# Performance work log

Hardware: AMD Instinct MI355X
Metric: run time of the kernel (lower is better)

Reference implementation:

```python
import math
import jax, jax.numpy as jnp
from jax import lax
import numpy as np

B, N, D, H, L, F = 128, 200, 128, 8, 3, 2048


def setup_inputs():
    key = jax.random.key(0)
    ks = jax.random.split(key, 24)
    g = lambda i, shape: (0.05 * jax.random.normal(ks[i], shape)).astype(jnp.float32)
    coords = jax.random.uniform(ks[0], (B, N, 2), dtype=jnp.float32)
    demands = jax.random.uniform(ks[1], (B, N), minval=1.0, maxval=10.0, dtype=jnp.float32)
    demands = demands.at[:, 0].set(0.0)  # depot demand = 0
    capacity = jnp.full((B,), 50.0, jnp.float32)
    return dict(
        coords=coords, demands_raw=demands, capacity_raw=capacity,
        embed_W=g(2, (D, 3)), embed_b=g(3, (D,)),
        Wqkv=g(4, (L, 3 * D, D)), bqkv=g(5, (L, 3 * D)),
        Wo=g(6, (L, D, D)), bo=g(7, (L, D)),
        W1=g(8, (L, F, D)), b1=g(9, (L, F)),
        W2=g(10, (L, D, F)), b2=g(11, (L, D)),
        ln1_g=jnp.ones((L, D), jnp.float32), ln1_b=jnp.zeros((L, D), jnp.float32),
        ln2_g=jnp.ones((L, D), jnp.float32), ln2_b=jnp.zeros((L, D), jnp.float32),
        Wq=g(12, (D, D)), Wk=g(13, (D, D)),
        Wcap=g(14, (D, 1)), bcap=g(15, (D,)),
        Wctx=g(16, (D, 3 * D)), bctx=g(17, (D,)),
    )


def _ln(x, g, b):
    m = x.mean(-1, keepdims=True)
    v = ((x - m) ** 2).mean(-1, keepdims=True)
    return (x - m) / jnp.sqrt(v + 1e-5) * g + b


def _forward(coords, demands_raw, capacity_raw, embed_W, embed_b, Wqkv, bqkv, Wo, bo,
             W1, b1, W2, b2, ln1_g, ln1_b, ln2_g, ln2_b, Wq, Wk, Wcap, bcap, Wctx, bctx):
    Bd, Nd, _ = coords.shape
    cap = capacity_raw.reshape(Bd, 1)
    demand_ratio = demands_raw / cap                       # (B,N)
    x = jnp.concatenate([coords, demand_ratio[..., None]], -1)  # (B,N,3)
    h = x @ embed_W.T + embed_b                            # (B,N,D)
    d = h.shape[-1]
    dh = d // H
    # --- transformer encoder (post-LN, relu FFN), eval mode (no dropout) ---
    for i in range(Wqkv.shape[0]):
        qkv = h @ Wqkv[i].T + bqkv[i]
        q, k, v = jnp.split(qkv, 3, -1)
        q = q.reshape(Bd, Nd, H, dh)
        k = k.reshape(Bd, Nd, H, dh)
        v = v.reshape(Bd, Nd, H, dh)
        s = jnp.einsum('bqhd,bkhd->bhqk', q, k) / math.sqrt(dh)
        a = jax.nn.softmax(s, -1)
        o = jnp.einsum('bhqk,bkhd->bqhd', a, v).reshape(Bd, Nd, d) @ Wo[i].T + bo[i]
        h = _ln(h + o, ln1_g[i], ln1_b[i])
        f = jax.nn.relu(h @ W1[i].T + b1[i]) @ W2[i].T + b2[i]
        h = _ln(h + f, ln2_g[i], ln2_b[i])
    global_ctx = h.mean(1)                                 # (B,D)
    kmat = h @ Wk.T                                        # K cache: static across steps
    sqrt_d = math.sqrt(d)
    max_steps = 2 * (Nd - 1) + 1
    ar = jnp.arange(Bd)

    def step(carry, _):
        current, visited, remaining, done, key = carry
        key, sk = jax.random.split(key)
        cur_h = h[ar, current]                             # (B,D)
        cap_h = remaining @ Wcap.T + bcap                  # (B,D)
        q_in = jnp.concatenate([cur_h, global_ctx, cap_h], -1)
        q = (q_in @ Wctx.T + bctx) @ Wq.T                  # (B,D)
        logits = (kmat * q[:, None, :]).sum(-1) / sqrt_d   # (B,N)
        infeasible = visited | (demand_ratio > remaining)
        feas_cust = (~visited[:, 1:]) & (demand_ratio[:, 1:] <= remaining)
        has_feas = feas_cust.any(1)
        all_served = visited[:, 1:].all(1)
        force_depot = all_served & (current != 0) & (~done)
        at_depot = (current == 0) & (~done)
        not_depot = (current != 0) & (~done)
        # prevent_early_return=True path
        depot_mask = (at_depot & has_feas) | (not_depot & has_feas & (~all_served))
        infeasible = infeasible.at[:, 0].set(infeasible[:, 0] | depot_mask)
        force_depot = force_depot | (not_depot & (~has_feas)) | done
        masked = jnp.where(infeasible, -1e9, logits)
        logp = jax.nn.log_softmax(masked, -1)
        sel = jax.random.categorical(sk, masked)           # sampling decode
        sel_logp = logp[ar, sel]
        sel = jnp.where(force_depot, 0, sel)
        sel_logp = jnp.where(force_depot, 0.0, sel_logp)
        is_depot = sel == 0
        take = demand_ratio[ar, sel][:, None]
        remaining = jnp.clip(jnp.where(is_depot[:, None], 1.0, remaining - take), 0.0, 1.0)
        visited = visited.at[ar, sel].set(visited[ar, sel] | (~is_depot))
        done = done | (visited[:, 1:].all(1) & (sel == 0))
        return (sel, visited, remaining, done, key), (sel, sel_logp)

    init = (jnp.zeros(Bd, jnp.int32), jnp.zeros((Bd, Nd), bool),
            jnp.ones((Bd, 1), coords.dtype), jnp.zeros(Bd, bool), jax.random.key(42))
    _, (acts, lps) = lax.scan(step, init, None, length=max_steps)
    path = jnp.concatenate([jnp.zeros((Bd, 1), jnp.int32), acts.T], 1)  # (B, 1+max_steps)
    logps = lps.sum(0)                                                  # (B,)
    return path, logps


def reference(coords, demands_raw, capacity_raw, embed_W, embed_b, Wqkv, bqkv, Wo, bo,
              W1, b1, W2, b2, ln1_g, ln1_b, ln2_g, ln2_b, Wq, Wk, Wcap, bcap, Wctx, bctx):
    return _forward(coords, demands_raw, capacity_raw, embed_W, embed_b, Wqkv, bqkv, Wo, bo,
                    W1, b1, W2, b2, ln1_g, ln1_b, ln2_g, ln2_b, Wq, Wk, Wcap, bcap, Wctx, bctx)
```

## Files before the change

kernel.cpp:

```cpp
#include <hip/hip_runtime.h>
#include <hip/hip_bf16.h>
#include <stdint.h>
#include <math.h>

#define NB 128
#define NN 200
#define ND 128
#define NH 8
#define DH 16
#define NL 3
#define NF 2048
#define NT (NB * NN)
#define NSTEP 399

__host__ __device__ inline void tf2x32(unsigned k0, unsigned k1, unsigned x0, unsigned x1,
                                       unsigned* o0, unsigned* o1) {
  unsigned ks[3] = {k0, k1, k0 ^ k1 ^ 0x1BD11BDAu};
  x0 += ks[0]; x1 += ks[1];
  const unsigned R[2][4] = {{13u, 15u, 26u, 6u}, {17u, 29u, 16u, 24u}};
#pragma unroll
  for (int i = 0; i < 5; ++i) {
#pragma unroll
    for (int j = 0; j < 4; ++j) {
      unsigned r = R[i & 1][j];
      x0 += x1;
      x1 = (x1 << r) | (x1 >> (32u - r));
      x1 ^= x0;
    }
    x0 += ks[(i + 1) % 3];
    x1 += ks[(i + 2) % 3] + (unsigned)(i + 1);
  }
  *o0 = x0; *o1 = x1;
}

__global__ void k_rng(unsigned* __restrict__ rng) {
  unsigned k0 = 0u, k1 = 42u;
  for (int t = 0; t < NSTEP; ++t) {
    unsigned a0, a1, s0, s1;
    tf2x32(k0, k1, 0u, 1u, &s0, &s1);
    tf2x32(k0, k1, 0u, 0u, &a0, &a1);
    rng[2 * t] = s0; rng[2 * t + 1] = s1;
    k0 = a0; k1 = a1;
  }
}

__global__ __launch_bounds__(256) void k_gum(const unsigned* __restrict__ rng, float* __restrict__ gum) {
  int idx = blockIdx.x * 256 + threadIdx.x;
  if (idx >= NSTEP * NT) return;
  int t = idx / NT, j = idx - t * NT;
  unsigned o0, o1;
  tf2x32(rng[2 * t], rng[2 * t + 1], 0u, (unsigned)j, &o0, &o1);
  unsigned bits = o0 ^ o1;
  float u01 = __uint_as_float((bits >> 9) | 0x3f800000u) - 1.0f;
  float uu = fmaxf(1.17549435082228751e-38f, u01);
  gum[idx] = (float)(-log(-log((double)uu)));
}

__global__ void k_tr(const float* __restrict__ src, float* __restrict__ dst, int R, int C) {
  int i = blockIdx.x * 256 + threadIdx.x;
  if (i >= R * C) return;
  int c = i / R, r = i - c * R;
  dst[i] = src[(size_t)r * C + c];
}

__global__ void k_trd(const float* __restrict__ src, double* __restrict__ dst, int R, int C) {
  int i = blockIdx.x * 256 + threadIdx.x;
  if (i >= R * C) return;
  int c = i / R, r = i - c * R;
  dst[i] = (double)src[(size_t)r * C + c];
}

__global__ void k_embed(const float* __restrict__ coords, const float* __restrict__ dem,
                        const float* __restrict__ cap, const float* __restrict__ eW,
                        const float* __restrict__ eb, float* __restrict__ h, float* __restrict__ dr) {
  int gid = blockIdx.x * blockDim.x + threadIdx.x;
  int t = gid >> 7, d = gid & 127;
  int b = t / NN;
  float drv = dem[t] / cap[b];
  double acc = (double)eW[d * 3] * (double)coords[2 * t]
             + (double)eW[d * 3 + 1] * (double)coords[2 * t + 1]
             + (double)eW[d * 3 + 2] * (double)drv;
  h[gid] = (float)acc + eb[d];
  if (d == 0) dr[t] = drv;
}

#define QT 8
__global__ __launch_bounds__(384) void k_qkv(const float* __restrict__ h, const double* __restrict__ WT,
                                             const float* __restrict__ bias, float* __restrict__ qkv) {
  const int t0 = blockIdx.x * QT, j = threadIdx.x;
  __shared__ double hsh[ND][QT];
  for (int idx = j; idx < ND * QT; idx += 384) {
    int t = idx & 7, k = idx >> 3;
    hsh[k][t] = (double)h[(size_t)(t0 + t) * ND + k];
  }
  __syncthreads();
  double acc[QT];
#pragma unroll
  for (int t = 0; t < QT; ++t) acc[t] = 0.0;
  for (int k = 0; k < ND; ++k) {
    double w = WT[(size_t)k * 384 + j];
#pragma unroll
    for (int t = 0; t < QT; ++t) acc[t] += w * hsh[k][t];
  }
  float bv = bias[j];
#pragma unroll
  for (int t = 0; t < QT; ++t)
    qkv[(size_t)(t0 + t) * 384 + j] = (float)acc[t] + bv;
}

__global__ __launch_bounds__(256) void k_attn(const float* __restrict__ qkv, float* __restrict__ att) {
  const int b = blockIdx.x / NH, hh = blockIdx.x % NH, tid = threadIdx.x;
  const int lane = tid & 63, w = tid >> 6;
  __shared__ float qsh[NN][DH + 1];
  __shared__ float ksh[NN][DH + 1];
  __shared__ float vsh[NN][DH + 1];
  __shared__ float ashw[4][NN + 8];
  for (int idx = tid; idx < NN * DH; idx += 256) {
    int n = idx / DH, d2 = idx % DH;
    size_t base = (size_t)(b * NN + n) * 384 + hh * DH + d2;
    qsh[n][d2] = qkv[base];
    ksh[n][d2] = qkv[base + ND];
    vsh[n][d2] = qkv[base + 2 * ND];
  }
  __syncthreads();
  const int dd = lane & 15, q4 = lane >> 4;
  for (int qn = w; qn < NN; qn += 4) {
    double qv[DH];
#pragma unroll
    for (int d = 0; d < DH; ++d) qv[d] = (double)qsh[qn][d];
    float sf[4];
#pragma unroll
    for (int s = 0; s < 4; ++s) {
      int n = lane + 64 * s;
      if (n < NN) {
        double a = 0.0;
#pragma unroll
        for (int d = 0; d < DH; ++d) a += qv[d] * (double)ksh[n][d];
        sf[s] = (float)a / 4.0f;
      } else sf[s] = -3.0e38f;
    }
    float m = fmaxf(fmaxf(sf[0], sf[1]), fmaxf(sf[2], sf[3]));
    for (int off = 1; off < 64; off <<= 1) m = fmaxf(m, __shfl_xor(m, off, 64));
    double e[4];
    double esum = 0.0;
#pragma unroll
    for (int s = 0; s < 4; ++s) {
      int n = lane + 64 * s;
      e[s] = (n < NN) ? exp((double)(sf[s] - m)) : 0.0;
      esum += e[s];
    }
    for (int off = 1; off < 64; off <<= 1) esum += __shfl_xor(esum, off, 64);
#pragma unroll
    for (int s = 0; s < 4; ++s) {
      int n = lane + 64 * s;
      if (n < NN) ashw[w][n] = (float)(e[s] / esum);
    }
    double o = 0.0;
    for (int i = 0; i < 50; ++i) {
      int n = q4 * 50 + i;
      o += (double)ashw[w][n] * (double)vsh[n][dd];
    }
    o += __shfl_xor(o, 16, 64);
    o += __shfl_xor(o, 32, 64);
    if (lane < DH)
      att[(size_t)(b * NN + qn) * ND + hh * DH + lane] = (float)o;
  }
}

#define OT 4
__global__ __launch_bounds__(128) void k_oln(const float* __restrict__ att, const double* __restrict__ WoT,
                                             const float* __restrict__ bo, const float* __restrict__ g,
                                             const float* __restrict__ bb, float* __restrict__ h) {
  const int t0 = blockIdx.x * OT, d = threadIdx.x;
  __shared__ double ash[ND][OT];
  __shared__ float xsh[OT][ND];
  __shared__ float mred[OT], sred[OT];
  for (int idx = d; idx < ND * OT; idx += 128) {
    int t = idx & 3, k = idx >> 2;
    ash[k][t] = (double)att[(size_t)(t0 + t) * ND + k];
  }
  __syncthreads();
  double acc[OT];
#pragma unroll
  for (int t = 0; t < OT; ++t) acc[t] = 0.0;
  for (int k = 0; k < ND; ++k) {
    double w = WoT[(size_t)k * ND + d];
#pragma unroll
    for (int t = 0; t < OT; ++t) acc[t] += w * ash[k][t];
  }
  float bv = bo[d];
#pragma unroll
  for (int t = 0; t < OT; ++t) {
    float o = (float)acc[t] + bv;
    xsh[t][d] = h[(size_t)(t0 + t) * ND + d] + o;
  }
  __syncthreads();
  if (d < OT) {
    double sv = 0.0;
    for (int k = 0; k < ND; ++k) sv += (double)xsh[d][k];
    float m = (float)(sv / 128.0);
    double sq = 0.0;
    for (int k = 0; k < ND; ++k) { float tf = xsh[d][k] - m; sq += (double)tf * (double)tf; }
    mred[d] = m;
    sred[d] = sqrtf((float)(sq / 128.0) + 1e-5f);
  }
  __syncthreads();
#pragma unroll
  for (int t = 0; t < OT; ++t) {
    float tf = xsh[t][d] - mred[t];
    h[(size_t)(t0 + t) * ND + d] = tf / sred[t] * g[d] + bb[d];
  }
}

#define FT 8
#define JC 1024
__global__ __launch_bounds__(256) void k_ffn(float* __restrict__ h, const double* __restrict__ W1T,
                                             const float* __restrict__ b1, const float* __restrict__ W2T,
                                             const float* __restrict__ b2, const float* __restrict__ g,
                                             const float* __restrict__ bb) {
  const int t0 = blockIdx.x * FT, tid = threadIdx.x;
  __shared__ double hsh[ND][FT];
  __shared__ double fsh[FT][JC];
  __shared__ float xsh[FT][ND];
  __shared__ float mred[FT], sred[FT];
  for (int idx = tid; idx < ND * FT; idx += 256) {
    int t = idx & 7, k = idx >> 3;
    hsh[k][t] = (double)h[(size_t)(t0 + t) * ND + k];
  }
  __syncthreads();
  const int jg = tid >> 5, dl = tid & 31;
  double acc2[4][FT];
#pragma unroll
  for (int a = 0; a < 4; ++a)
#pragma unroll
    for (int t = 0; t < FT; ++t) acc2[a][t] = 0.0;
  for (int c = 0; c < 2; ++c) {
    {
      const int j0 = tid * 4;
      double acc[4][FT];
#pragma unroll
      for (int a = 0; a < 4; ++a)
#pragma unroll
        for (int t = 0; t < FT; ++t) acc[a][t] = 0.0;
      for (int k = 0; k < ND; ++k) {
        double hv[FT];
#pragma unroll
        for (int t = 0; t < FT; ++t) hv[t] = hsh[k][t];
        const double* wp = W1T + (size_t)k * NF + c * JC + j0;
        double2 wa = *(const double2*)wp;
        double2 wb = *(const double2*)(wp + 2);
        double wd[4] = {wa.x, wa.y, wb.x, wb.y};
#pragma unroll
        for (int a = 0; a < 4; ++a)
#pragma unroll
          for (int t = 0; t < FT; ++t) acc[a][t] += wd[a] * hv[t];
      }
#pragma unroll
      for (int a = 0; a < 4; ++a) {
        float bv = b1[c * JC + j0 + a];
#pragma unroll
        for (int t = 0; t < FT; ++t) {
          float f = (float)acc[a][t] + bv;
          fsh[t][j0 + a] = (double)fmaxf(f, 0.0f);
        }
      }
    }
    __syncthreads();
    for (int i = 0; i < 128; ++i) {
      int jj = (jg << 7) | ((i + jg) & 127);
      int j = c * JC + jj;
      double fv[FT];
#pragma unroll
      for (int t = 0; t < FT; ++t) fv[t] = fsh[t][jj];
      float4 wv = *(const float4*)(W2T + (size_t)j * ND + (dl << 2));
      double wd[4] = {(double)wv.x, (double)wv.y, (double)wv.z, (double)wv.w};
#pragma unroll
      for (int a = 0; a < 4; ++a)
#pragma unroll
        for (int t = 0; t < FT; ++t) acc2[a][t] += wd[a] * fv[t];
    }
    __syncthreads();
  }
  double* red = &fsh[0][0];
#pragma unroll
  for (int a = 0; a < 4; ++a)
#pragma unroll
    for (int t = 0; t < FT; ++t)
      red[(((jg * 8 + t) << 7)) + (dl << 2) + a] = acc2[a][t];
  __syncthreads();
  for (int idx = tid; idx < ND * FT; idx += 256) {
    int t = idx >> 7, d = idx & 127;
    double s = 0.0;
#pragma unroll
    for (int jg2 = 0; jg2 < 8; ++jg2) s += red[((jg2 * 8 + t) << 7) + d];
    float o = (float)s + b2[d];
    float hf = (float)hsh[d][t];
    xsh[t][d] = hf + o;
  }
  __syncthreads();
  if (tid < FT) {
    double sv = 0.0;
    for (int d = 0; d < ND; ++d) sv += (double)xsh[tid][d];
    float m = (float)(sv / 128.0);
    double sq = 0.0;
    for (int d = 0; d < ND; ++d) { float tf = xsh[tid][d] - m; sq += (double)tf * (double)tf; }
    mred[tid] = m;
    sred[tid] = sqrtf((float)(sq / 128.0) + 1e-5f);
  }
  __syncthreads();
  for (int idx = tid; idx < ND * FT; idx += 256) {
    int d = idx & 127, t = idx >> 7;
    float tf = xsh[t][d] - mred[t];
    h[(size_t)(t0 + t) * ND + d] = tf / sred[t] * g[d] + bb[d];
  }
}

__global__ __launch_bounds__(128) void k_gctx(const float* __restrict__ h, float* __restrict__ gctx) {
  int b = blockIdx.x, d = threadIdx.x;
  double acc = 0.0;
  for (int n = 0; n < NN; ++n) acc += (double)h[(size_t)(b * NN + n) * ND + d];
  gctx[b * ND + d] = (float)(acc / 200.0);
}

#define KT 8
__global__ __launch_bounds__(128) void k_kmat(const float* __restrict__ h, const double* __restrict__ WkT,
                                              float* __restrict__ kmat) {
  const int t0 = blockIdx.x * KT, d = threadIdx.x;
  __shared__ double hsh[ND][KT];
  for (int idx = d; idx < ND * KT; idx += 128) {
    int t = idx & 7, k = idx >> 3;
    hsh[k][t] = (double)h[(size_t)(t0 + t) * ND + k];
  }
  __syncthreads();
  double acc[KT];
#pragma unroll
  for (int t = 0; t < KT; ++t) acc[t] = 0.0;
  for (int k = 0; k < ND; ++k) {
    double w = WkT[(size_t)k * ND + d];
#pragma unroll
    for (int t = 0; t < KT; ++t) acc[t] += w * hsh[k][t];
  }
#pragma unroll
  for (int t = 0; t < KT; ++t)
    kmat[(size_t)(t0 + t) * ND + d] = (float)acc[t];
}

__global__ __launch_bounds__(128) void k_prep1(const float* __restrict__ Wctx, const float* __restrict__ bcap,
                                               const float* __restrict__ Wcap, const float* __restrict__ bctx,
                                               double* __restrict__ t1, double* __restrict__ wu) {
  int k = threadIdx.x;
  double a = 0.0, c = 0.0;
  for (int m = 0; m < ND; ++m) {
    double wc = (double)Wctx[(size_t)k * 384 + 256 + m];
    a += wc * (double)bcap[m];
    c += wc * (double)Wcap[m];
  }
  t1[k] = a + (double)bctx[k];
  wu[k] = c;
}

__global__ __launch_bounds__(128) void k_M(const float* __restrict__ Wq, const float* __restrict__ Wctx,
                                           double* __restrict__ M) {
  int d = blockIdx.x, j = threadIdx.x;
  double acc = 0.0;
  for (int k = 0; k < ND; ++k)
    acc += (double)Wq[(size_t)d * ND + k] * (double)Wctx[(size_t)k * 384 + j];
  M[(size_t)d * ND + j] = acc;
}

__global__ __launch_bounds__(128) void k_u(const float* __restrict__ Wq, const double* __restrict__ wu,
                                           double* __restrict__ u) {
  int d = threadIdx.x;
  double acc = 0.0;
  for (int k = 0; k < ND; ++k) acc += (double)Wq[(size_t)d * ND + k] * wu[k];
  u[d] = acc;
}

__global__ __launch_bounds__(128) void k_t2(const float* __restrict__ Wctx, const float* __restrict__ gctx,
                                            double* __restrict__ t2) {
  int b = blockIdx.x, k = threadIdx.x;
  double acc = 0.0;
  for (int m = 0; m < ND; ++m)
    acc += (double)Wctx[(size_t)k * 384 + 128 + m] * (double)gctx[b * ND + m];
  t2[(size_t)b * ND + k] = acc;
}

__global__ __launch_bounds__(128) void k_vb(const float* __restrict__ Wq, const double* __restrict__ t2,
                                            const double* __restrict__ t1, double* __restrict__ vb) {
  int b = blockIdx.x, d = threadIdx.x;
  double acc = 0.0;
  for (int k = 0; k < ND; ++k)
    acc += (double)Wq[(size_t)d * ND + k] * (t2[(size_t)b * ND + k] + t1[k]);
  vb[(size_t)b * ND + d] = acc;
}

__global__ __launch_bounds__(256) void k_c01(const float* __restrict__ kmat, const double* __restrict__ vb,
                                             const double* __restrict__ u, float* __restrict__ c0, float* __restrict__ c1) {
  int t = blockIdx.x * 256 + threadIdx.x;
  if (t >= NT) return;
  int b = t / NN;
  double a0 = 0.0, a1 = 0.0;
  for (int d = 0; d < ND; ++d) {
    double km = (double)kmat[(size_t)t * ND + d];
    a0 += km * vb[(size_t)b * ND + d];
    a1 += km * u[d];
  }
  c0[t] = (float)a0;
  c1[t] = (float)a1;
}

__global__ __launch_bounds__(128) void k_KM(const float* __restrict__ kmat, const double* __restrict__ M,
                                            float* __restrict__ KMT) {
  const int t0 = blockIdx.x * KT, j = threadIdx.x;
  const int b = t0 / NN, toff = t0 % NN;
  __shared__ double ksh[ND][KT];
  for (int idx = j; idx < ND * KT; idx += 128) {
    int t = idx & 7, k = idx >> 3;
    ksh[k][t] = (double)kmat[(size_t)(t0 + t) * ND + k];
  }
  __syncthreads();
  double acc[KT];
#pragma unroll
  for (int t = 0; t < KT; ++t) acc[t] = 0.0;
  for (int d = 0; d < ND; ++d) {
    double m = M[(size_t)d * ND + j];
#pragma unroll
    for (int t = 0; t < KT; ++t) acc[t] += ksh[d][t] * m;
  }
#pragma unroll
  for (int t = 0; t < KT; ++t)
    KMT[(size_t)b * ND * NN + (size_t)j * NN + toff + t] = (float)acc[t];
}

#define PC 8
__global__ __launch_bounds__(256) void k_P(const float* __restrict__ KMT, const float* __restrict__ h,
                                           float* __restrict__ P) {
  const int blk = blockIdx.x;
  const int b = blk / 25, c0 = (blk % 25) * PC;
  const int tid = threadIdx.x;
  __shared__ double h8[ND][PC];
  for (int idx = tid; idx < ND * PC; idx += 256) {
    int t = idx & 7, j = idx >> 3;
    h8[j][t] = (double)h[(size_t)(b * NN + c0 + t) * ND + j];
  }
  __syncthreads();
  if (tid < NN) {
    double acc[PC];
#pragma unroll
    for (int t = 0; t < PC; ++t) acc[t] = 0.0;
    const float* kb = KMT + (size_t)b * ND * NN + tid;
    for (int j = 0; j < ND; ++j) {
      double km = (double)kb[(size_t)j * NN];
#pragma unroll
      for (int t = 0; t < PC; ++t) acc[t] += km * h8[j][t];
    }
#pragma unroll
    for (int t = 0; t < PC; ++t)
      P[(size_t)(b * NN + c0 + t) * NN + tid] = (float)acc[t];
  }
}

__global__ __launch_bounds__(64) void k_decode(const float* __restrict__ P, const float* __restrict__ c0,
                                               const float* __restrict__ c1, const float* __restrict__ dr,
                                               const float* __restrict__ gum, float* __restrict__ out) {
  __shared__ float Psh[NN * NN];
  const int b = blockIdx.x, l = threadIdx.x;
  {
    const float4* src = (const float4*)(P + (size_t)b * NN * NN);
    float4* dst = (float4*)Psh;
    for (int i = l; i < (NN * NN) / 4; i += 64) dst[i] = src[i];
  }
  float drs4[4], c04[4], c14[4];
  int vis4[4];
#pragma unroll
  for (int s = 0; s < 4; ++s) {
    int n = l + 64 * s;
    bool valid = n < NN;
    drs4[s] = valid ? dr[b * NN + n] : 1e9f;
    c04[s] = valid ? c0[b * NN + n] : 0.0f;
    c14[s] = valid ? c1[b * NN + n] : 0.0f;
    vis4[s] = valid ? 0 : 1;
  }
  int cur = 0, done = 0;
  float rem = 1.0f, lpsum = 0.0f;
  if (l == 0) out[(size_t)b * 400] = 0.0f;
  __syncthreads();
  const float SQD = 11.3137084989847603f;
  float gv4[4];
#pragma unroll
  for (int s = 0; s < 4; ++s) {
    int n = l + 64 * s;
    gv4[s] = (n < NN) ? gum[(size_t)0 * NT + b * NN + n] : 0.0f;
  }
  for (int t = 0; t < NSTEP; ++t) {
    float gn4[4];
    if (t + 1 < NSTEP) {
      const float* grow = gum + (size_t)(t + 1) * NT + b * NN;
#pragma unroll
      for (int s = 0; s < 4; ++s) {
        int n = l + 64 * s;
        gn4[s] = (n < NN) ? grow[n] : 0.0f;
      }
    }
    const float* Prow = Psh + cur * NN;
    float Pv4[4];
#pragma unroll
    for (int s = 0; s < 4; ++s) {
      int n = l + 64 * s;
      Pv4[s] = (n < NN) ? Prow[n] : 0.0f;
    }
    bool lf = false, lns = false;
#pragma unroll
    for (int s = 0; s < 4; ++s) {
      int n = l + 64 * s;
      if (n >= 1 && n < NN && !vis4[s]) {
        lns = true;
        if (drs4[s] <= rem) lf = true;
      }
    }
    const int has_feas = (__ballot(lf) != 0ULL);
    const int all_served = (__ballot(lns) == 0ULL);
    const bool at_depot = (cur == 0) && !done, not_depot = (cur != 0) && !done;
    const bool depot_mask = (at_depot && has_feas) || (not_depot && has_feas && !all_served);
    float msk[4], sc[4];
#pragma unroll
    for (int s = 0; s < 4; ++s) {
      int n = l + 64 * s;
      if (n < NN) {
        double sd = (double)Pv4[s] + (double)c04[s] + (double)rem * (double)c14[s];
        float logit = (float)sd / SQD;
        bool infn = vis4[s] || (drs4[s] > rem) || (n == 0 && depot_mask);
        msk[s] = infn ? -1e9f : logit;
        sc[s] = msk[s] + gv4[s];
      } else {
        msk[s] = -3.0e38f;
        sc[s] = -3.0e38f;
      }
    }
    float bs = sc[0]; int bn = l; float bmsk = msk[0]; float mx = msk[0];
#pragma unroll
    for (int s = 1; s < 4; ++s) {
      int n = l + 64 * s;
      if (sc[s] > bs) { bs = sc[s]; bn = n; bmsk = msk[s]; }
      mx = fmaxf(mx, msk[s]);
    }
    for (int off = 1; off < 64; off <<= 1) {
      float os = __shfl_xor(bs, off, 64);
      int on = __shfl_xor(bn, off, 64);
      float ob = __shfl_xor(bmsk, off, 64);
      float om = __shfl_xor(mx, off, 64);
      if (os > bs || (os == bs && on < bn)) { bs = os; bn = on; bmsk = ob; }
      mx = fmaxf(mx, om);
    }
    float e = 0.0f;
#pragma unroll
    for (int s = 0; s < 4; ++s) e += expf(msk[s] - mx);
    for (int off = 1; off < 64; off <<= 1) e += __shfl_xor(e, off, 64);
    int sel = bn;
    float slp = (bmsk - mx) - logf(e);
    bool force = (all_served && cur != 0 && !done) || (not_depot && !has_feas) || done;
    if (force) { sel = 0; slp = 0.0f; }
    if (l == 0) out[(size_t)b * 400 + 1 + t] = (float)sel;
    lpsum += slp;
    bool isd = (sel == 0);
    float cand = drs4[sel >> 6];
    float take = __shfl(cand, sel & 63, 64);
    float nr = isd ? 1.0f : (rem - take);
    rem = fminf(fmaxf(nr, 0.0f), 1.0f);
    if (!isd && (sel & 63) == l) vis4[sel >> 6] = 1;
    if (all_served && sel == 0) done = 1;
    cur = sel;
#pragma unroll
    for (int s = 0; s < 4; ++s) gv4[s] = gn4[s];
  }
  if (l == 0) out[(size_t)NB * 400 + b] = lpsum;
}

extern "C" void kernel_launch(void* const* d_in, const int* in_sizes, int n_in,
                              void* d_out, int out_size, void* d_ws, size_t ws_size,
                              hipStream_t stream) {
  (void)in_sizes; (void)n_in; (void)out_size; (void)ws_size;
  const float* coords = (const float*)d_in[0];
  const float* dem    = (const float*)d_in[1];
  const float* cap    = (const float*)d_in[2];
  const float* eW     = (const float*)d_in[3];
  const float* eb     = (const float*)d_in[4];
  const float* Wqkv   = (const float*)d_in[5];
  const float* bqkv   = (const float*)d_in[6];
  const float* Wo     = (const float*)d_in[7];
  const float* bo     = (const float*)d_in[8];
  const float* W1     = (const float*)d_in[9];
  const float* b1     = (const float*)d_in[10];
  const float* W2     = (const float*)d_in[11];
  const float* b2     = (const float*)d_in[12];
  const float* ln1g   = (const float*)d_in[13];
  const float* ln1b   = (const float*)d_in[14];
  const float* ln2g   = (const float*)d_in[15];
  const float* ln2b   = (const float*)d_in[16];
  const float* Wq     = (const float*)d_in[17];
  const float* Wk     = (const float*)d_in[18];
  const float* Wcap   = (const float*)d_in[19];
  const float* bcap   = (const float*)d_in[20];
  const float* Wctx   = (const float*)d_in[21];
  const float* bctx   = (const float*)d_in[22];

  char* ws = (char*)d_ws;
  size_t off = 0;
  auto take = [&](size_t bytes) -> void* {
    void* p = ws + off;
    off += (bytes + 255) & ~(size_t)255;
    return p;
  };
  float* dr   = (float*)take((size_t)NT * 4);
  float* c0   = (float*)take((size_t)NT * 4);
  float* c1   = (float*)take((size_t)NT * 4);
  float* P    = (float*)take((size_t)NB * NN * NN * 4);
  unsigned* rng = (unsigned*)take((size_t)NSTEP * 2 * 4);
  float* h    = (float*)take((size_t)NT * ND * 4);
  float* qkv  = (float*)take((size_t)NT * 384 * 4);
  float* att  = (float*)take((size_t)NT * ND * 4);
  float* kmat = (float*)take((size_t)NT * ND * 4);
  float* gctx = (float*)take((size_t)NB * ND * 4);
  double* M   = (double*)take((size_t)ND * ND * 8);
  double* u   = (double*)take((size_t)ND * 8);
  double* t1  = (double*)take((size_t)ND * 8);
  double* wu  = (double*)take((size_t)ND * 8);
  double* t2  = (double*)take((size_t)NB * ND * 8);
  double* vb  = (double*)take((size_t)NB * ND * 8);
  double* W1T   = (double*)take((size_t)NL * NF * ND * 8);
  float*  W2T   = (float*)take((size_t)NL * NF * ND * 4);
  double* WqkvT = (double*)take((size_t)NL * 384 * ND * 8);
  double* WoT   = (double*)take((size_t)NL * ND * ND * 8);
  double* WkT   = (double*)take((size_t)ND * ND * 8);
  float* KMT = qkv;
  float* gum = h;

  k_rng<<<1, 1, 0, stream>>>(rng);
  for (int i = 0; i < NL; ++i) {
    k_trd<<<(NF * ND + 255) / 256, 256, 0, stream>>>(W1 + (size_t)i * NF * ND, W1T + (size_t)i * NF * ND, NF, ND);
    k_tr<<<(NF * ND + 255) / 256, 256, 0, stream>>>(W2 + (size_t)i * ND * NF, W2T + (size_t)i * ND * NF, ND, NF);
    k_trd<<<(384 * ND + 255) / 256, 256, 0, stream>>>(Wqkv + (size_t)i * 384 * ND, WqkvT + (size_t)i * 384 * ND, 384, ND);
    k_trd<<<(ND * ND + 255) / 256, 256, 0, stream>>>(Wo + (size_t)i * ND * ND, WoT + (size_t)i * ND * ND, ND, ND);
  }
  k_trd<<<(ND * ND + 255) / 256, 256, 0, stream>>>(Wk, WkT, ND, ND);
  k_embed<<<(NT * ND) / 256, 256, 0, stream>>>(coords, dem, cap, eW, eb, h, dr);
  for (int i = 0; i < NL; ++i) {
    k_qkv<<<NT / QT, 384, 0, stream>>>(h, WqkvT + (size_t)i * 384 * ND, bqkv + (size_t)i * 384, qkv);
    k_attn<<<NB * NH, 256, 0, stream>>>(qkv, att);
    k_oln<<<NT / OT, 128, 0, stream>>>(att, WoT + (size_t)i * ND * ND, bo + (size_t)i * ND,
                                       ln1g + (size_t)i * ND, ln1b + (size_t)i * ND, h);
    k_ffn<<<NT / FT, 256, 0, stream>>>(h, W1T + (size_t)i * NF * ND, b1 + (size_t)i * NF,
                                       W2T + (size_t)i * ND * NF, b2 + (size_t)i * ND,
                                       ln2g + (size_t)i * ND, ln2b + (size_t)i * ND);
  }
  k_gctx<<<NB, 128, 0, stream>>>(h, gctx);
  k_kmat<<<NT / KT, 128, 0, stream>>>(h, WkT, kmat);
  k_prep1<<<1, 128, 0, stream>>>(Wctx, bcap, Wcap, bctx, t1, wu);
  k_M<<<ND, 128, 0, stream>>>(Wq, Wctx, M);
  k_u<<<1, 128, 0, stream>>>(Wq, wu, u);
  k_t2<<<NB, 128, 0, stream>>>(Wctx, gctx, t2);
  k_vb<<<NB, 128, 0, stream>>>(Wq, t2, t1, vb);
  k_c01<<<NT / 256, 256, 0, stream>>>(kmat, vb, u, c0, c1);
  k_KM<<<NT / KT, 128, 0, stream>>>(kmat, M, KMT);
  k_P<<<NB * 25, 256, 0, stream>>>(KMT, h, P);
  k_gum<<<(NSTEP * NT + 255) / 256, 256, 0, stream>>>(rng, gum);
  k_decode<<<NB, 64, 0, stream>>>(P, c0, c1, dr, gum, (float*)d_out);
}
```

Measured before the change: 4.746 ms.

## Halve FFN shared memory, prefetch FFN weights, parallelize RNG key splitting

The FFN kernel now stores the ReLU intermediate in shared memory as float instead of double, halving that buffer (64KB to 32KB), and splits the cross-group reduction into two halves so it fits in the smaller buffer. This should allow more blocks to be resident per CU. Both FFN inner loops software-prefetch the next weight row into registers to hide global-load latency, at the cost of extra registers. The RNG kernel computes the sequential key chain on one thread and then spreads the per-step subkey derivation across 64 threads.

Result: no change. 4.747 ms (+0.0%).

```diff
diff --git a/kernel.cpp b/kernel.cpp
--- a/kernel.cpp
+++ b/kernel.cpp
@@ -34,13 +34,22 @@
 }
 
 __global__ void k_rng(unsigned* __restrict__ rng) {
-  unsigned k0 = 0u, k1 = 42u;
-  for (int t = 0; t < NSTEP; ++t) {
-    unsigned a0, a1, s0, s1;
-    tf2x32(k0, k1, 0u, 1u, &s0, &s1);
-    tf2x32(k0, k1, 0u, 0u, &a0, &a1);
+  __shared__ unsigned ksh[2 * NSTEP];
+  const int l = threadIdx.x;
+  if (l == 0) {
+    unsigned k0 = 0u, k1 = 42u;
+    for (int t = 0; t < NSTEP; ++t) {
+      ksh[2 * t] = k0; ksh[2 * t + 1] = k1;
+      unsigned a0, a1;
+      tf2x32(k0, k1, 0u, 0u, &a0, &a1);
+      k0 = a0; k1 = a1;
+    }
+  }
+  __syncthreads();
+  for (int t = l; t < NSTEP; t += 64) {
+    unsigned s0, s1;
+    tf2x32(ksh[2 * t], ksh[2 * t + 1], 0u, 1u, &s0, &s1);
     rng[2 * t] = s0; rng[2 * t + 1] = s1;
-    k0 = a0; k1 = a1;
   }
 }
 
@@ -220,9 +229,10 @@
                                              const float* __restrict__ bb) {
   const int t0 = blockIdx.x * FT, tid = threadIdx.x;
   __shared__ double hsh[ND][FT];
-  __shared__ double fsh[FT][JC];
+  __shared__ double fsh_raw[FT * JC / 2];
   __shared__ float xsh[FT][ND];
   __shared__ float mred[FT], sred[FT];
+  float* fshf = (float*)fsh_raw;
   for (int idx = tid; idx < ND * FT; idx += 256) {
     int t = idx & 7, k = idx >> 3;
     hsh[k][t] = (double)h[(size_t)(t0 + t) * ND + k];
@@ -242,14 +252,17 @@
       for (int a = 0; a < 4; ++a)
 #pragma unroll
         for (int t = 0; t < FT; ++t) acc[a][t] = 0.0;
+      const double* wp0 = W1T + (size_t)c * JC + j0;
+      double2 wa = *(const double2*)wp0;
+      double2 wb = *(const double2*)(wp0 + 2);
       for (int k = 0; k < ND; ++k) {
+        double wd[4] = {wa.x, wa.y, wb.x, wb.y};
+        const double* wn = W1T + (size_t)((k + 1) & 127) * NF + c * JC + j0;
+        wa = *(const double2*)wn;
+        wb = *(const double2*)(wn + 2);
         double hv[FT];
 #pragma unroll
         for (int t = 0; t < FT; ++t) hv[t] = hsh[k][t];
-        const double* wp = W1T + (size_t)k * NF + c * JC + j0;
-        double2 wa = *(const double2*)wp;
-        double2 wb = *(const double2*)(wp + 2);
-        double wd[4] = {wa.x, wa.y, wb.x, wb.y};
 #pragma unroll
         for (int a = 0; a < 4; ++a)
 #pragma unroll
@@ -261,41 +274,48 @@
 #pragma unroll
         for (int t = 0; t < FT; ++t) {
           float f = (float)acc[a][t] + bv;
-          fsh[t][j0 + a] = (double)fmaxf(f, 0.0f);
+          fshf[t * JC + j0 + a] = fmaxf(f, 0.0f);
         }
       }
     }
     __syncthreads();
-    for (int i = 0; i < 128; ++i) {
-      int jj = (jg << 7) | ((i + jg) & 127);
-      int j = c * JC + jj;
-      double fv[FT];
-#pragma unroll
-      for (int t = 0; t < FT; ++t) fv[t] = fsh[t][jj];
-      float4 wv = *(const float4*)(W2T + (size_t)j * ND + (dl << 2));
-      double wd[4] = {(double)wv.x, (double)wv.y, (double)wv.z, (double)wv.w};
-#pragma unroll
-      for (int a = 0; a < 4; ++a)
-#pragma unroll
-        for (int t = 0; t < FT; ++t) acc2[a][t] += wd[a] * fv[t];
+    {
+      float4 wv = *(const float4*)(W2T + (size_t)(c * JC + ((jg << 7) | (jg & 127))) * ND + (dl << 2));
+      for (int i = 0; i < 128; ++i) {
+        int jj = (jg << 7) | ((i + jg) & 127);
+        int jn = (jg << 7) | ((i + 1 + jg) & 127);
+        float4 wnext = *(const float4*)(W2T + (size_t)(c * JC + jn) * ND + (dl << 2));
+        double fv[FT];
+#pragma unroll
+        for (int t = 0; t < FT; ++t) fv[t] = (double)fshf[t * JC + jj];
+        double wd[4] = {(double)wv.x, (double)wv.y, (double)wv.z, (double)wv.w};
+#pragma unroll
+        for (int a = 0; a < 4; ++a)
+#pragma unroll
+          for (int t = 0; t < FT; ++t) acc2[a][t] += wd[a] * fv[t];
+        wv = wnext;
+      }
     }
     __syncthreads();
   }
-  double* red = &fsh[0][0];
-#pragma unroll
-  for (int a = 0; a < 4; ++a)
-#pragma unroll
-    for (int t = 0; t < FT; ++t)
-      red[(((jg * 8 + t) << 7)) + (dl << 2) + a] = acc2[a][t];
-  __syncthreads();
-  for (int idx = tid; idx < ND * FT; idx += 256) {
-    int t = idx >> 7, d = idx & 127;
-    double s = 0.0;
-#pragma unroll
-    for (int jg2 = 0; jg2 < 8; ++jg2) s += red[((jg2 * 8 + t) << 7) + d];
-    float o = (float)s + b2[d];
-    float hf = (float)hsh[d][t];
-    xsh[t][d] = hf + o;
+  double* red = fsh_raw;
+  for (int half = 0; half < 2; ++half) {
+    if (half) __syncthreads();
+#pragma unroll
+    for (int a = 0; a < 4; ++a)
+#pragma unroll
+      for (int t = 0; t < 4; ++t)
+        red[((jg * 4 + t) << 7) + (dl << 2) + a] = acc2[a][half * 4 + t];
+    __syncthreads();
+    for (int idx = tid; idx < ND * 4; idx += 256) {
+      int t = idx >> 7, d = idx & 127;
+      double s = 0.0;
+#pragma unroll
+      for (int jg2 = 0; jg2 < 8; ++jg2) s += red[((jg2 * 4 + t) << 7) + d];
+      float o = (float)s + b2[d];
+      int tt = half * 4 + t;
+      xsh[tt][d] = (float)hsh[d][tt] + o;
+    }
   }
   __syncthreads();
   if (tid < FT) {
@@ -635,7 +655,7 @@
   float* KMT = qkv;
   float* gum = h;
 
-  k_rng<<<1, 1, 0, stream>>>(rng);
+  k_rng<<<1, 64, 0, stream>>>(rng);
   for (int i = 0; i < NL; ++i) {
     k_trd<<<(NF * ND + 255) / 256, 256, 0, stream>>>(W1 + (size_t)i * NF * ND, W1T + (size_t)i * NF * ND, NF, ND);
     k_tr<<<(NF * ND + 255) / 256, 256, 0, stream>>>(W2 + (size_t)i * ND * NF, W2T + (size_t)i * ND * NF, ND, NF);
```
